# Kernel optimization log

Measured on AMD Instinct MI355X. Metric: run time of the kernel, lower is better.

The kernel has to match this reference:

```python
import jax, jax.numpy as jnp
import numpy as np

NUM_HEADS = 16
NUM_GROUPS = 4
GROUP_SIZE = NUM_HEADS // NUM_GROUPS
EMB_DIM = 1024
HEAD_DIM = EMB_DIM // NUM_HEADS
BLOCK_SIZE = 2048
B, T = 4, 2048


def setup_inputs() -> dict:
    key = jax.random.key(0)
    ks = jax.random.split(key, 7)
    s = 0.02
    x = jax.random.normal(ks[0], (B, T, EMB_DIM), dtype=jnp.float32)
    # nn.Linear weights are [out_features, in_features]; stacked per head/group
    Wq = jax.random.normal(ks[1], (NUM_HEADS, HEAD_DIM, EMB_DIM), dtype=jnp.float32) * s
    Wk = jax.random.normal(ks[2], (NUM_GROUPS, HEAD_DIM, EMB_DIM), dtype=jnp.float32) * s
    Wv = jax.random.normal(ks[3], (NUM_GROUPS, HEAD_DIM, EMB_DIM), dtype=jnp.float32) * s
    Wp = jax.random.normal(ks[4], (EMB_DIM, EMB_DIM), dtype=jnp.float32) * s
    bp = jax.random.normal(ks[5], (EMB_DIM,), dtype=jnp.float32) * s
    return {"x": x, "Wq": Wq, "Wk": Wk, "Wv": Wv, "Wp": Wp, "bp": bp}


def reference(x, Wq, Wk, Wv, Wp, bp):
    # Dropout is treated as identity (eval mode) for a deterministic baseline.
    b, t, c = x.shape
    # per-head queries: [b, t, H, d]
    q = jnp.einsum('btc,hdc->bthd', x, Wq)
    # per-group keys/values: [b, t, G, d]
    k = jnp.einsum('btc,gdc->btgd', x, Wk)
    v = jnp.einsum('btc,gdc->btgd', x, Wv)
    # expand groups to heads: head h uses group h // GROUP_SIZE
    k = jnp.repeat(k, GROUP_SIZE, axis=2)  # [b, t, H, d]
    v = jnp.repeat(v, GROUP_SIZE, axis=2)
    scale = HEAD_DIM ** (-0.5)
    scores = jnp.einsum('bqhd,bkhd->bhqk', q, k) * scale  # [b, H, t, t]
    causal = jnp.tril(jnp.ones((t, t), dtype=bool))
    scores = jnp.where(causal, scores, -jnp.inf)
    p = jax.nn.softmax(scores, axis=-1)
    out = jnp.einsum('bhqk,bkhd->bqhd', p, v)  # [b, t, H, d]
    out = out.reshape(b, t, c)  # concat heads in head-index order
    return out @ Wp.T + bp
```

## Files before the change

### kernel.cpp

```cpp
#include <hip/hip_runtime.h>

typedef unsigned short u16;
typedef __bf16 bf16_t;
typedef bf16_t bf16x8 __attribute__((ext_vector_type(8)));
typedef float f32x4 __attribute__((ext_vector_type(4)));
typedef u16 u16x8 __attribute__((ext_vector_type(8)));

#define T_SZ 2048
#define EMB 1024

static __device__ __forceinline__ u16 f2bf(float f) {
  union { float f; unsigned u; } v; v.f = f;
  return (u16)((v.u + 0x7fffu + ((v.u >> 16) & 1u)) >> 16);
}
static __device__ __forceinline__ unsigned cvtpk(float a, float b) {
  unsigned r;
  asm("v_cvt_pk_bf16_f32 %0, %1, %2" : "=v"(r) : "v"(a), "v"(b));
  return r;
}
static __device__ __forceinline__ void async16(const u16* g, u16* l) {
  typedef const __attribute__((address_space(1))) unsigned int* gp_t;
  typedef __attribute__((address_space(3))) unsigned int* lp_t;
  __builtin_amdgcn_global_load_lds((gp_t)(const void*)g, (lp_t)(void*)l, 16, 0, 0);
}

__global__ __launch_bounds__(256) void cvt_all(
    const float* __restrict__ x,  const float* __restrict__ Wq,
    const float* __restrict__ Wk, const float* __restrict__ Wv,
    const float* __restrict__ Wp, u16* __restrict__ xb, u16* __restrict__ Wqb,
    u16* __restrict__ Wkb, u16* __restrict__ Wvb, u16* __restrict__ Wpb) {
  int bid = blockIdx.x;
  const float* src; u16* dst; int off;
  if (bid < 4096)      { src = x;  dst = xb;  off = bid * 2048; }
  else if (bid < 4608) { src = Wq; dst = Wqb; off = (bid - 4096) * 2048; }
  else if (bid < 4736) { src = Wk; dst = Wkb; off = (bid - 4608) * 2048; }
  else if (bid < 4864) { src = Wv; dst = Wvb; off = (bid - 4736) * 2048; }
  else                 { src = Wp; dst = Wpb; off = (bid - 4864) * 2048; }
  int i = off + threadIdx.x * 8;
  float4 a = *(const float4*)(src + i);
  float4 b = *(const float4*)(src + i + 4);
  u16x8 o;
  o[0] = f2bf(a.x); o[1] = f2bf(a.y); o[2] = f2bf(a.z); o[3] = f2bf(a.w);
  o[4] = f2bf(b.x); o[5] = f2bf(b.y); o[6] = f2bf(b.z); o[7] = f2bf(b.w);
  *(u16x8*)(dst + i) = o;
}

__global__ __launch_bounds__(256) void transpose_v(
    const u16* __restrict__ V, u16* __restrict__ Vt) {
  __shared__ u16 tile[64][72];
  const int tt = blockIdx.x, g = blockIdx.y, b = blockIdx.z;
  const int tid = threadIdx.x;
  {
    const int r = tid >> 2, c = (tid & 3) * 16;
    const u16* src = V + ((size_t)(b * T_SZ + tt * 64 + r)) * 256 + g * 64 + c;
    *(u16x8*)&tile[r][c] = *(const u16x8*)src;
    *(u16x8*)&tile[r][c + 8] = *(const u16x8*)(src + 8);
  }
  __syncthreads();
  {
    const int d = tid >> 2, t0 = (tid & 3) * 16;
    u16x8 o0, o1;
#pragma unroll
    for (int i = 0; i < 8; ++i) { o0[i] = tile[t0 + i][d]; o1[i] = tile[t0 + 8 + i][d]; }
    u16* dst = Vt + ((size_t)((b * 4 + g) * 64 + d)) * T_SZ + tt * 64 + t0;
    *(u16x8*)dst = o0;
    *(u16x8*)(dst + 8) = o1;
  }
}

template <bool OUT_F32>
__device__ __forceinline__ void gemm_body(
    const u16* __restrict__ A, const u16* __restrict__ Bm,
    const float* __restrict__ bias, void* __restrict__ Cv,
    int N, int K, int tm, int tn, float cmul) {
  __shared__ u16 as[128 * 64];
  __shared__ u16 bs[128 * 64];
  const int tid = threadIdx.x;
  const int lane = tid & 63, wv = tid >> 6;
  const int quad = lane >> 4, l16 = lane & 15;
  const int wm = (wv & 1) * 64, wn = (wv >> 1) * 64;
  const int rA = lane >> 3;
  const int cS = ((lane & 7) ^ (rA & 7)) * 8;
  const int x7 = l16 & 7;
  f32x4 acc[4][4] = {};
  for (int k0 = 0; k0 < K; k0 += 64) {
#pragma unroll
    for (int it = 0; it < 4; ++it) {
      int r0 = it * 32 + wv * 8;
      async16(A + (size_t)(tm + r0 + rA) * K + k0 + cS, &as[r0 * 64]);
      async16(Bm + (size_t)(tn + r0 + rA) * K + k0 + cS, &bs[r0 * 64]);
    }
    __syncthreads();
#pragma unroll
    for (int kk = 0; kk < 64; kk += 32) {
      const int cb = kk >> 3;
      bf16x8 af[4], bfr[4];
#pragma unroll
      for (int i = 0; i < 4; ++i)
        af[i] = *(const bf16x8*)&as[(wm + i * 16 + l16) * 64 + (((cb + quad) ^ x7) * 8)];
#pragma unroll
      for (int j = 0; j < 4; ++j)
        bfr[j] = *(const bf16x8*)&bs[(wn + j * 16 + l16) * 64 + (((cb + quad) ^ x7) * 8)];
#pragma unroll
      for (int i = 0; i < 4; ++i)
#pragma unroll
        for (int j = 0; j < 4; ++j)
          acc[i][j] = __builtin_amdgcn_mfma_f32_16x16x32_bf16(af[i], bfr[j], acc[i][j], 0, 0, 0);
    }
    __syncthreads();
  }
#pragma unroll
  for (int i = 0; i < 4; ++i)
#pragma unroll
    for (int j = 0; j < 4; ++j) {
      int col = tn + wn + j * 16 + l16;
      float bv = bias ? bias[col] : 0.0f;
#pragma unroll
      for (int r = 0; r < 4; ++r) {
        int row = tm + wm + i * 16 + quad * 4 + r;
        if (OUT_F32)
          ((float*)Cv)[(size_t)row * N + col] = acc[i][j][r] + bv;
        else
          ((u16*)Cv)[(size_t)row * N + col] = f2bf(acc[i][j][r] * cmul + bv);
      }
    }
}

__global__ __launch_bounds__(256, 2) void gemm_qkv(
    const u16* __restrict__ x, const u16* __restrict__ Wq,
    const u16* __restrict__ Wk, const u16* __restrict__ Wv,
    u16* __restrict__ Qb, u16* __restrict__ Kb, u16* __restrict__ Vb) {
  const int y = blockIdx.y;
  const u16* Bm; u16* C; int N, tn; float cm;
  const float SCALE2 = 0.18033688011112042f;
  if (y < 8)       { Bm = Wq; C = Qb; N = 1024; tn = y * 128;        cm = SCALE2; }
  else if (y < 10) { Bm = Wk; C = Kb; N = 256;  tn = (y - 8) * 128;  cm = 1.0f; }
  else             { Bm = Wv; C = Vb; N = 256;  tn = (y - 10) * 128; cm = 1.0f; }
  gemm_body<false>(x, Bm, nullptr, C, N, 1024, blockIdx.x * 128, tn, cm);
}

__global__ __launch_bounds__(256, 2) void gemm_out(
    const u16* __restrict__ A, const u16* __restrict__ Wp,
    const float* __restrict__ bias, float* __restrict__ C) {
  gemm_body<true>(A, Wp, bias, C, 1024, 1024, blockIdx.x * 128, blockIdx.y * 128, 1.0f);
}

__global__ __launch_bounds__(512, 6) void gqa_attn(
    const u16* __restrict__ Q, const u16* __restrict__ Kg,
    const u16* __restrict__ Vt, u16* __restrict__ O) {
  __shared__ u16 kbuf[3][64 * 64];
  __shared__ u16 vbuf[3][64 * 64];
  __shared__ u16 pls[8][16 * 72];
  const int tid = threadIdx.x;
  const int lane = tid & 63, wv = tid >> 6;
  const int quad = lane >> 4, l16 = lane & 15;
  const int bid = blockIdx.x;
  const int xcd = bid & 7, slot = bid >> 3;
  const int pr = slot & 7, u2 = slot >> 3;
  const int bg = xcd + 8 * (u2 & 1);
  const int b = bg >> 2, g = bg & 3;
  const int h = g * 4 + (u2 >> 1);
  const size_t bT = (size_t)b * T_SZ;
  const int rA = lane >> 3;
  const int cS = ((lane & 7) ^ (rA & 7)) * 8;
  const int x7 = l16 & 7;
  const u16* vtb = Vt + (size_t)((b * 4 + g) * 64) * T_SZ;

#define STAGE(KT, BUF)                                                              \
  do {                                                                              \
    int kb_ = (KT) * 64, r0_ = wv * 8;                   \
    async16(Kg + (bT + kb_ + r0_ + rA) * 256 + g * 64 + cS, &kbuf[BUF][r0_ * 64]);  \
    async16(vtb + (size_t)(r0_ + rA) * T_SZ + kb_ + cS, &vbuf[BUF][r0_ * 64]);      \
    __builtin_amdgcn_sched_barrier(0);                                              \
  } while (0)

  for (int pass = 0; pass < 2; ++pass) {
    const int qt = pass ? pr : 15 - pr;
    const int qstrip = qt * 128 + wv * 16;
    const int nkt = 2 * qt + 2;

    const u16* qp = Q + (bT + qstrip + l16) * EMB + h * 64 + quad * 8;
    const bf16x8 qf0 = *(const bf16x8*)qp;
    const bf16x8 qf1 = *(const bf16x8*)(qp + 32);

    f32x4 o[4] = {};
    float l_p = 0.0f;

    __syncthreads();
    STAGE(0, 0);
    STAGE(1, 1);
    for (int kt = 0; kt < nkt; ++kt) {
      if (kt < nkt - 1) { asm volatile("s_waitcnt vmcnt(2)" ::: "memory"); }
      else              { asm volatile("s_waitcnt vmcnt(0)" ::: "memory"); }
      __builtin_amdgcn_s_barrier();
      if (kt + 2 < nkt) STAGE(kt + 2, (kt + 2) % 3);
      const int cur = kt % 3;
      const int kb = kt * 64;
      const bool act = (kb <= qstrip + 15);

      if (act) {
        f32x4 s4[4];
        __builtin_amdgcn_s_setprio(1);
#pragma unroll
        for (int jn = 0; jn < 4; ++jn) {
          const int rowb = (jn * 16 + l16) * 64;
          bf16x8 kf0 = *(const bf16x8*)&kbuf[cur][rowb + ((quad ^ x7) * 8)];
          bf16x8 kf1 = *(const bf16x8*)&kbuf[cur][rowb + (((4 + quad) ^ x7) * 8)];
          f32x4 a = {};
          a = __builtin_amdgcn_mfma_f32_16x16x32_bf16(kf0, qf0, a, 0, 0, 0);
          a = __builtin_amdgcn_mfma_f32_16x16x32_bf16(kf1, qf1, a, 0, 0, 0);
          s4[jn] = a;
        }
        __builtin_amdgcn_s_setprio(0);
        if (kb + 63 > qstrip) {
          const int qg = qstrip + l16;
#pragma unroll
          for (int jn = 0; jn < 4; ++jn)
#pragma unroll
            for (int r = 0; r < 4; ++r)
              if (kb + jn * 16 + quad * 4 + r > qg) s4[jn][r] = -1e30f;
        }
        float sj[4];
#pragma unroll
        for (int jn = 0; jn < 4; ++jn) {
#pragma unroll
          for (int r = 0; r < 4; ++r) s4[jn][r] = exp2f(s4[jn][r]);
          sj[jn] = (s4[jn][0] + s4[jn][1]) + (s4[jn][2] + s4[jn][3]);
        }
        l_p += (sj[0] + sj[1]) + (sj[2] + sj[3]);
#pragma unroll
        for (int jn = 0; jn < 4; ++jn) {
          uint2 w;
          w.x = cvtpk(s4[jn][0], s4[jn][1]);
          w.y = cvtpk(s4[jn][2], s4[jn][3]);
          *(uint2*)&pls[wv][l16 * 72 + jn * 16 + quad * 4] = w;
        }
        bf16x8 pf0 = *(const bf16x8*)&pls[wv][l16 * 72 + quad * 8];
        bf16x8 pf1 = *(const bf16x8*)&pls[wv][l16 * 72 + 32 + quad * 8];
        __builtin_amdgcn_s_setprio(1);
#pragma unroll
        for (int j = 0; j < 4; ++j) {
          const int rowb = (j * 16 + l16) * 64;
          bf16x8 vf0 = *(const bf16x8*)&vbuf[cur][rowb + ((quad ^ x7) * 8)];
          bf16x8 vf1 = *(const bf16x8*)&vbuf[cur][rowb + (((4 + quad) ^ x7) * 8)];
          o[j] = __builtin_amdgcn_mfma_f32_16x16x32_bf16(pf0, vf0, o[j], 0, 0, 0);
          o[j] = __builtin_amdgcn_mfma_f32_16x16x32_bf16(pf1, vf1, o[j], 0, 0, 0);
        }
        __builtin_amdgcn_s_setprio(0);
      }
    }
    float l_l = l_p;
    l_l += __shfl_xor(l_l, 16);
    l_l += __shfl_xor(l_l, 32);
#pragma unroll
    for (int r = 0; r < 4; ++r) {
      float inv = 1.0f / __shfl(l_l, quad * 4 + r, 16);
      int row = qstrip + quad * 4 + r;
#pragma unroll
      for (int j = 0; j < 4; ++j)
        O[(bT + row) * EMB + h * 64 + j * 16 + l16] = f2bf(o[j][r] * inv);
    }
  }
#undef STAGE
}

extern "C" void kernel_launch(void* const* d_in, const int* in_sizes, int n_in,
                              void* d_out, int out_size, void* d_ws, size_t ws_size,
                              hipStream_t stream) {
  const float* x  = (const float*)d_in[0];
  const float* Wq = (const float*)d_in[1];
  const float* Wk = (const float*)d_in[2];
  const float* Wv = (const float*)d_in[3];
  const float* Wp = (const float*)d_in[4];
  const float* bp = (const float*)d_in[5];
  float* out = (float*)d_out;

  u16* ws = (u16*)d_ws;
  u16* Qb  = ws;
  u16* Kb  = Qb + (size_t)8192 * 1024;
  u16* Vb  = Kb + (size_t)8192 * 256;
  u16* Vtb = Vb + (size_t)8192 * 256;
  u16* xb  = Vtb + (size_t)8192 * 256;
  u16* Wqb = xb + (size_t)8192 * 1024;
  u16* Wkb = Wqb + (size_t)1024 * 1024;
  u16* Wvb = Wkb + (size_t)256 * 1024;
  u16* Wpb = Wvb + (size_t)256 * 1024;
  u16* Ab  = xb;

  cvt_all<<<dim3(5376), 256, 0, stream>>>(x, Wq, Wk, Wv, Wp, xb, Wqb, Wkb, Wvb, Wpb);
  gemm_qkv<<<dim3(64, 12), 256, 0, stream>>>(xb, Wqb, Wkb, Wvb, Qb, Kb, Vb);
  transpose_v<<<dim3(32, 4, 4), 256, 0, stream>>>(Vb, Vtb);
  gqa_attn<<<dim3(512), 512, 0, stream>>>(Qb, Kb, Vtb, Ab);
  gemm_out<<<dim3(64, 8), 256, 0, stream>>>(Ab, Wpb, bp, out);
}
```

Measured before the change: 207.5 us.

## Shrink attention blocks to 64-row query tiles with double buffering and swizzled P

The attention kernel now uses 256-thread blocks, each owning a 64-row query tile, launched as 1024 blocks instead of 512. The triple-buffered K/V pipeline with explicit vmcnt waits becomes a double-buffered one with a __syncthreads per step. The P staging buffer switches from padded rows to an XOR-swizzled layout. Since each wave now always has at least one unmasked key tile, the per-tile activity check goes away, removing idle causal work and improving load balance and occupancy. In exchange, each loaded K/V tile is shared by fewer waves and the shallower pipeline may expose more load latency.

```diff
diff --git a/kernel.cpp b/kernel.cpp
--- a/kernel.cpp
+++ b/kernel.cpp
@@ -145,39 +145,46 @@
   gemm_body<true>(A, Wp, bias, C, 1024, 1024, blockIdx.x * 128, blockIdx.y * 128, 1.0f);
 }
 
-__global__ __launch_bounds__(512, 6) void gqa_attn(
+__global__ __launch_bounds__(256, 4) void gqa_attn(
     const u16* __restrict__ Q, const u16* __restrict__ Kg,
     const u16* __restrict__ Vt, u16* __restrict__ O) {
-  __shared__ u16 kbuf[3][64 * 64];
-  __shared__ u16 vbuf[3][64 * 64];
-  __shared__ u16 pls[8][16 * 72];
+  __shared__ u16 kbuf[2][64 * 64];
+  __shared__ u16 vbuf[2][64 * 64];
+  __shared__ u16 pls[4][16 * 64];
   const int tid = threadIdx.x;
   const int lane = tid & 63, wv = tid >> 6;
   const int quad = lane >> 4, l16 = lane & 15;
   const int bid = blockIdx.x;
-  const int xcd = bid & 7, slot = bid >> 3;
-  const int pr = slot & 7, u2 = slot >> 3;
-  const int bg = xcd + 8 * (u2 & 1);
+  const int xcd = bid & 7;
+  const int slot = (bid >> 3) & 31;
+  const int w = bid >> 8;
+  const int pr = slot & 15;
+  const int bg = xcd + 8 * (w & 1);
   const int b = bg >> 2, g = bg & 3;
-  const int h = g * 4 + (u2 >> 1);
+  const int h = g * 4 + (slot >> 4) + 2 * (w >> 1);
   const size_t bT = (size_t)b * T_SZ;
   const int rA = lane >> 3;
   const int cS = ((lane & 7) ^ (rA & 7)) * 8;
   const int x7 = l16 & 7;
   const u16* vtb = Vt + (size_t)((b * 4 + g) * 64) * T_SZ;
-
-#define STAGE(KT, BUF)                                                              \
-  do {                                                                              \
-    int kb_ = (KT) * 64, r0_ = wv * 8;                   \
-    async16(Kg + (bT + kb_ + r0_ + rA) * 256 + g * 64 + cS, &kbuf[BUF][r0_ * 64]);  \
-    async16(vtb + (size_t)(r0_ + rA) * T_SZ + kb_ + cS, &vbuf[BUF][r0_ * 64]);      \
-    __builtin_amdgcn_sched_barrier(0);                                              \
+  char* pw = (char*)pls + wv * 2048 + l16 * 128;
+
+#define STAGE(KT, BUF)                                                               \
+  do {                                                                               \
+    int kb_ = (KT) * 64, r0_ = wv * 16;                  \
+    async16(Kg + (bT + kb_ + r0_ + rA) * 256 + g * 64 + cS, &kbuf[BUF][r0_ * 64]);   \
+    async16(Kg + (bT + kb_ + r0_ + 8 + rA) * 256 + g * 64 + cS,                      \
+            &kbuf[BUF][(r0_ + 8) * 64]);                                             \
+    async16(vtb + (size_t)(r0_ + rA) * T_SZ + kb_ + cS, &vbuf[BUF][r0_ * 64]);       \
+    async16(vtb + (size_t)(r0_ + 8 + rA) * T_SZ + kb_ + cS,                          \
+            &vbuf[BUF][(r0_ + 8) * 64]);                                             \
+    __builtin_amdgcn_sched_barrier(0);                                               \
   } while (0)
 
   for (int pass = 0; pass < 2; ++pass) {
-    const int qt = pass ? pr : 15 - pr;
-    const int qstrip = qt * 128 + wv * 16;
-    const int nkt = 2 * qt + 2;
+    const int qs = pass ? pr : 31 - pr;
+    const int qstrip = qs * 64 + wv * 16;
+    const int nkt = qs + 1;
 
     const u16* qp = Q + (bT + qstrip + l16) * EMB + h * 64 + quad * 8;
     const bf16x8 qf0 = *(const bf16x8*)qp;
@@ -188,66 +195,60 @@
 
     __syncthreads();
     STAGE(0, 0);
-    STAGE(1, 1);
     for (int kt = 0; kt < nkt; ++kt) {
-      if (kt < nkt - 1) { asm volatile("s_waitcnt vmcnt(2)" ::: "memory"); }
-      else              { asm volatile("s_waitcnt vmcnt(0)" ::: "memory"); }
-      __builtin_amdgcn_s_barrier();
-      if (kt + 2 < nkt) STAGE(kt + 2, (kt + 2) % 3);
-      const int cur = kt % 3;
+      const int cur = kt & 1;
+      __syncthreads();
+      if (kt + 1 < nkt) STAGE(kt + 1, cur ^ 1);
       const int kb = kt * 64;
-      const bool act = (kb <= qstrip + 15);
-
-      if (act) {
-        f32x4 s4[4];
-        __builtin_amdgcn_s_setprio(1);
-#pragma unroll
-        for (int jn = 0; jn < 4; ++jn) {
-          const int rowb = (jn * 16 + l16) * 64;
-          bf16x8 kf0 = *(const bf16x8*)&kbuf[cur][rowb + ((quad ^ x7) * 8)];
-          bf16x8 kf1 = *(const bf16x8*)&kbuf[cur][rowb + (((4 + quad) ^ x7) * 8)];
-          f32x4 a = {};
-          a = __builtin_amdgcn_mfma_f32_16x16x32_bf16(kf0, qf0, a, 0, 0, 0);
-          a = __builtin_amdgcn_mfma_f32_16x16x32_bf16(kf1, qf1, a, 0, 0, 0);
-          s4[jn] = a;
-        }
-        __builtin_amdgcn_s_setprio(0);
-        if (kb + 63 > qstrip) {
-          const int qg = qstrip + l16;
-#pragma unroll
-          for (int jn = 0; jn < 4; ++jn)
-#pragma unroll
-            for (int r = 0; r < 4; ++r)
-              if (kb + jn * 16 + quad * 4 + r > qg) s4[jn][r] = -1e30f;
-        }
-        float sj[4];
-#pragma unroll
-        for (int jn = 0; jn < 4; ++jn) {
-#pragma unroll
-          for (int r = 0; r < 4; ++r) s4[jn][r] = exp2f(s4[jn][r]);
-          sj[jn] = (s4[jn][0] + s4[jn][1]) + (s4[jn][2] + s4[jn][3]);
-        }
-        l_p += (sj[0] + sj[1]) + (sj[2] + sj[3]);
-#pragma unroll
-        for (int jn = 0; jn < 4; ++jn) {
-          uint2 w;
-          w.x = cvtpk(s4[jn][0], s4[jn][1]);
-          w.y = cvtpk(s4[jn][2], s4[jn][3]);
-          *(uint2*)&pls[wv][l16 * 72 + jn * 16 + quad * 4] = w;
-        }
-        bf16x8 pf0 = *(const bf16x8*)&pls[wv][l16 * 72 + quad * 8];
-        bf16x8 pf1 = *(const bf16x8*)&pls[wv][l16 * 72 + 32 + quad * 8];
-        __builtin_amdgcn_s_setprio(1);
-#pragma unroll
-        for (int j = 0; j < 4; ++j) {
-          const int rowb = (j * 16 + l16) * 64;
-          bf16x8 vf0 = *(const bf16x8*)&vbuf[cur][rowb + ((quad ^ x7) * 8)];
-          bf16x8 vf1 = *(const bf16x8*)&vbuf[cur][rowb + (((4 + quad) ^ x7) * 8)];
-          o[j] = __builtin_amdgcn_mfma_f32_16x16x32_bf16(pf0, vf0, o[j], 0, 0, 0);
-          o[j] = __builtin_amdgcn_mfma_f32_16x16x32_bf16(pf1, vf1, o[j], 0, 0, 0);
-        }
-        __builtin_amdgcn_s_setprio(0);
-      }
+
+      f32x4 s4[4];
+      __builtin_amdgcn_s_setprio(1);
+#pragma unroll
+      for (int jn = 0; jn < 4; ++jn) {
+        const int rowb = (jn * 16 + l16) * 64;
+        bf16x8 kf0 = *(const bf16x8*)&kbuf[cur][rowb + ((quad ^ x7) * 8)];
+        bf16x8 kf1 = *(const bf16x8*)&kbuf[cur][rowb + (((4 + quad) ^ x7) * 8)];
+        f32x4 a = {};
+        a = __builtin_amdgcn_mfma_f32_16x16x32_bf16(kf0, qf0, a, 0, 0, 0);
+        a = __builtin_amdgcn_mfma_f32_16x16x32_bf16(kf1, qf1, a, 0, 0, 0);
+        s4[jn] = a;
+      }
+      __builtin_amdgcn_s_setprio(0);
+      if (kb + 63 > qstrip) {
+        const int qg = qstrip + l16;
+#pragma unroll
+        for (int jn = 0; jn < 4; ++jn)
+#pragma unroll
+          for (int r = 0; r < 4; ++r)
+            if (kb + jn * 16 + quad * 4 + r > qg) s4[jn][r] = -1e30f;
+      }
+      float sj[4];
+#pragma unroll
+      for (int jn = 0; jn < 4; ++jn) {
+#pragma unroll
+        for (int r = 0; r < 4; ++r) s4[jn][r] = exp2f(s4[jn][r]);
+        sj[jn] = (s4[jn][0] + s4[jn][1]) + (s4[jn][2] + s4[jn][3]);
+      }
+      l_p += (sj[0] + sj[1]) + (sj[2] + sj[3]);
+#pragma unroll
+      for (int jn = 0; jn < 4; ++jn) {
+        uint2 wq;
+        wq.x = cvtpk(s4[jn][0], s4[jn][1]);
+        wq.y = cvtpk(s4[jn][2], s4[jn][3]);
+        *(uint2*)(pw + ((((jn * 2 + (quad >> 1)) ^ x7) * 16) | ((quad & 1) * 8))) = wq;
+      }
+      bf16x8 pf0 = *(const bf16x8*)(pw + ((quad ^ x7) * 16));
+      bf16x8 pf1 = *(const bf16x8*)(pw + (((4 + quad) ^ x7) * 16));
+      __builtin_amdgcn_s_setprio(1);
+#pragma unroll
+      for (int j = 0; j < 4; ++j) {
+        const int rowb = (j * 16 + l16) * 64;
+        bf16x8 vf0 = *(const bf16x8*)&vbuf[cur][rowb + ((quad ^ x7) * 8)];
+        bf16x8 vf1 = *(const bf16x8*)&vbuf[cur][rowb + (((4 + quad) ^ x7) * 8)];
+        o[j] = __builtin_amdgcn_mfma_f32_16x16x32_bf16(pf0, vf0, o[j], 0, 0, 0);
+        o[j] = __builtin_amdgcn_mfma_f32_16x16x32_bf16(pf1, vf1, o[j], 0, 0, 0);
+      }
+      __builtin_amdgcn_s_setprio(0);
     }
     float l_l = l_p;
     l_l += __shfl_xor(l_l, 16);
@@ -290,6 +291,6 @@
   cvt_all<<<dim3(5376), 256, 0, stream>>>(x, Wq, Wk, Wv, Wp, xb, Wqb, Wkb, Wvb, Wpb);
   gemm_qkv<<<dim3(64, 12), 256, 0, stream>>>(xb, Wqb, Wkb, Wvb, Qb, Kb, Vb);
   transpose_v<<<dim3(32, 4, 4), 256, 0, stream>>>(Vb, Vtb);
-  gqa_attn<<<dim3(512), 512, 0, stream>>>(Qb, Kb, Vtb, Ab);
+  gqa_attn<<<dim3(1024), 256, 0, stream>>>(Qb, Kb, Vtb, Ab);
   gemm_out<<<dim3(64, 8), 256, 0, stream>>>(Ab, Wpb, bp, out);
 }
```

Result: slower. 220.9 us (+6.5%).

## Process two 16-row query tiles per wave to reuse K/V fragments

Applied to the files above, without the earlier changes.

Each wave now handles 32 query rows (two 16-row MFMA tiles) instead of 16, so every K and V fragment read from LDS feeds twice as many MFMAs. The block tiling moves from 128-row to 256-row query strips with a new workgroup-to-strip mapping, replacing the two-pass causal pairing loop. The three-stage LDS ring becomes a double buffer, and launch bounds occupancy drops from 6 to 4. In exchange it uses more registers, gives each wave less lookahead in the pipeline, and produces larger and fewer blocks, which may hurt causal load balance. The launch grid code is not shown, so it is unclear whether it was updated to match the new block count.

```diff
diff --git a/kernel.cpp b/kernel.cpp
--- a/kernel.cpp
+++ b/kernel.cpp
@@ -145,21 +145,24 @@
   gemm_body<true>(A, Wp, bias, C, 1024, 1024, blockIdx.x * 128, blockIdx.y * 128, 1.0f);
 }
 
-__global__ __launch_bounds__(512, 6) void gqa_attn(
+__global__ __launch_bounds__(512, 4) void gqa_attn(
     const u16* __restrict__ Q, const u16* __restrict__ Kg,
     const u16* __restrict__ Vt, u16* __restrict__ O) {
-  __shared__ u16 kbuf[3][64 * 64];
-  __shared__ u16 vbuf[3][64 * 64];
-  __shared__ u16 pls[8][16 * 72];
+  __shared__ u16 kbuf[2][64 * 64];
+  __shared__ u16 vbuf[2][64 * 64];
+  __shared__ u16 pls[8][32 * 72];
   const int tid = threadIdx.x;
   const int lane = tid & 63, wv = tid >> 6;
   const int quad = lane >> 4, l16 = lane & 15;
   const int bid = blockIdx.x;
-  const int xcd = bid & 7, slot = bid >> 3;
-  const int pr = slot & 7, u2 = slot >> 3;
-  const int bg = xcd + 8 * (u2 & 1);
+  const int xcd = bid & 7, slot = (bid >> 3) & 31, w = bid >> 8;
+  const int bg = xcd + 8 * (slot & 1);
   const int b = bg >> 2, g = bg & 3;
-  const int h = g * 4 + (u2 >> 1);
+  const int h = g * 4 + ((slot >> 1) & 3);
+  const int c = (slot >> 3) & 3;
+  const int qs = w ? 7 - c : c;
+  const int nkt = 4 * qs + 4;
+  const int qstrip = qs * 256 + wv * 32;
   const size_t bT = (size_t)b * T_SZ;
   const int rA = lane >> 3;
   const int cS = ((lane & 7) ^ (rA & 7)) * 8;
@@ -174,94 +177,111 @@
     __builtin_amdgcn_sched_barrier(0);                                              \
   } while (0)
 
-  for (int pass = 0; pass < 2; ++pass) {
-    const int qt = pass ? pr : 15 - pr;
-    const int qstrip = qt * 128 + wv * 16;
-    const int nkt = 2 * qt + 2;
-
-    const u16* qp = Q + (bT + qstrip + l16) * EMB + h * 64 + quad * 8;
-    const bf16x8 qf0 = *(const bf16x8*)qp;
-    const bf16x8 qf1 = *(const bf16x8*)(qp + 32);
-
-    f32x4 o[4] = {};
-    float l_p = 0.0f;
-
+  const u16* qpa = Q + (bT + qstrip + l16) * EMB + h * 64 + quad * 8;
+  const u16* qpb = qpa + 16 * EMB;
+  const bf16x8 qf0a = *(const bf16x8*)qpa;
+  const bf16x8 qf1a = *(const bf16x8*)(qpa + 32);
+  const bf16x8 qf0b = *(const bf16x8*)qpb;
+  const bf16x8 qf1b = *(const bf16x8*)(qpb + 32);
+
+  f32x4 oa[4] = {}, ob[4] = {};
+  float lpa = 0.0f, lpb = 0.0f;
+
+  STAGE(0, 0);
+  for (int kt = 0; kt < nkt; ++kt) {
+    const int cur = kt & 1;
     __syncthreads();
-    STAGE(0, 0);
-    STAGE(1, 1);
-    for (int kt = 0; kt < nkt; ++kt) {
-      if (kt < nkt - 1) { asm volatile("s_waitcnt vmcnt(2)" ::: "memory"); }
-      else              { asm volatile("s_waitcnt vmcnt(0)" ::: "memory"); }
-      __builtin_amdgcn_s_barrier();
-      if (kt + 2 < nkt) STAGE(kt + 2, (kt + 2) % 3);
-      const int cur = kt % 3;
-      const int kb = kt * 64;
-      const bool act = (kb <= qstrip + 15);
-
-      if (act) {
-        f32x4 s4[4];
-        __builtin_amdgcn_s_setprio(1);
-#pragma unroll
-        for (int jn = 0; jn < 4; ++jn) {
-          const int rowb = (jn * 16 + l16) * 64;
-          bf16x8 kf0 = *(const bf16x8*)&kbuf[cur][rowb + ((quad ^ x7) * 8)];
-          bf16x8 kf1 = *(const bf16x8*)&kbuf[cur][rowb + (((4 + quad) ^ x7) * 8)];
-          f32x4 a = {};
-          a = __builtin_amdgcn_mfma_f32_16x16x32_bf16(kf0, qf0, a, 0, 0, 0);
-          a = __builtin_amdgcn_mfma_f32_16x16x32_bf16(kf1, qf1, a, 0, 0, 0);
-          s4[jn] = a;
+    if (kt + 1 < nkt) STAGE(kt + 1, cur ^ 1);
+    const int kb = kt * 64;
+    const bool act = (kb <= qstrip + 31);
+
+    if (act) {
+      f32x4 sa[4], sb[4];
+      __builtin_amdgcn_s_setprio(1);
+#pragma unroll
+      for (int jn = 0; jn < 4; ++jn) {
+        const int rowb = (jn * 16 + l16) * 64;
+        bf16x8 kf0 = *(const bf16x8*)&kbuf[cur][rowb + ((quad ^ x7) * 8)];
+        bf16x8 kf1 = *(const bf16x8*)&kbuf[cur][rowb + (((4 + quad) ^ x7) * 8)];
+        f32x4 a = {};
+        a = __builtin_amdgcn_mfma_f32_16x16x32_bf16(kf0, qf0a, a, 0, 0, 0);
+        a = __builtin_amdgcn_mfma_f32_16x16x32_bf16(kf1, qf1a, a, 0, 0, 0);
+        sa[jn] = a;
+        f32x4 bacc = {};
+        bacc = __builtin_amdgcn_mfma_f32_16x16x32_bf16(kf0, qf0b, bacc, 0, 0, 0);
+        bacc = __builtin_amdgcn_mfma_f32_16x16x32_bf16(kf1, qf1b, bacc, 0, 0, 0);
+        sb[jn] = bacc;
+      }
+      __builtin_amdgcn_s_setprio(0);
+      if (kb + 63 > qstrip) {
+        const int qga = qstrip + l16, qgb = qstrip + 16 + l16;
+#pragma unroll
+        for (int jn = 0; jn < 4; ++jn)
+#pragma unroll
+          for (int r = 0; r < 4; ++r) {
+            int kp = kb + jn * 16 + quad * 4 + r;
+            if (kp > qga) sa[jn][r] = -1e30f;
+            if (kp > qgb) sb[jn][r] = -1e30f;
+          }
+      }
+      float sja[4], sjb[4];
+#pragma unroll
+      for (int jn = 0; jn < 4; ++jn) {
+#pragma unroll
+        for (int r = 0; r < 4; ++r) {
+          sa[jn][r] = exp2f(sa[jn][r]);
+          sb[jn][r] = exp2f(sb[jn][r]);
         }
-        __builtin_amdgcn_s_setprio(0);
-        if (kb + 63 > qstrip) {
-          const int qg = qstrip + l16;
-#pragma unroll
-          for (int jn = 0; jn < 4; ++jn)
-#pragma unroll
-            for (int r = 0; r < 4; ++r)
-              if (kb + jn * 16 + quad * 4 + r > qg) s4[jn][r] = -1e30f;
-        }
-        float sj[4];
-#pragma unroll
-        for (int jn = 0; jn < 4; ++jn) {
-#pragma unroll
-          for (int r = 0; r < 4; ++r) s4[jn][r] = exp2f(s4[jn][r]);
-          sj[jn] = (s4[jn][0] + s4[jn][1]) + (s4[jn][2] + s4[jn][3]);
-        }
-        l_p += (sj[0] + sj[1]) + (sj[2] + sj[3]);
-#pragma unroll
-        for (int jn = 0; jn < 4; ++jn) {
-          uint2 w;
-          w.x = cvtpk(s4[jn][0], s4[jn][1]);
-          w.y = cvtpk(s4[jn][2], s4[jn][3]);
-          *(uint2*)&pls[wv][l16 * 72 + jn * 16 + quad * 4] = w;
-        }
-        bf16x8 pf0 = *(const bf16x8*)&pls[wv][l16 * 72 + quad * 8];
-        bf16x8 pf1 = *(const bf16x8*)&pls[wv][l16 * 72 + 32 + quad * 8];
-        __builtin_amdgcn_s_setprio(1);
-#pragma unroll
-        for (int j = 0; j < 4; ++j) {
-          const int rowb = (j * 16 + l16) * 64;
-          bf16x8 vf0 = *(const bf16x8*)&vbuf[cur][rowb + ((quad ^ x7) * 8)];
-          bf16x8 vf1 = *(const bf16x8*)&vbuf[cur][rowb + (((4 + quad) ^ x7) * 8)];
-          o[j] = __builtin_amdgcn_mfma_f32_16x16x32_bf16(pf0, vf0, o[j], 0, 0, 0);
-          o[j] = __builtin_amdgcn_mfma_f32_16x16x32_bf16(pf1, vf1, o[j], 0, 0, 0);
-        }
-        __builtin_amdgcn_s_setprio(0);
-      }
-    }
-    float l_l = l_p;
-    l_l += __shfl_xor(l_l, 16);
-    l_l += __shfl_xor(l_l, 32);
-#pragma unroll
-    for (int r = 0; r < 4; ++r) {
-      float inv = 1.0f / __shfl(l_l, quad * 4 + r, 16);
-      int row = qstrip + quad * 4 + r;
-#pragma unroll
-      for (int j = 0; j < 4; ++j)
-        O[(bT + row) * EMB + h * 64 + j * 16 + l16] = f2bf(o[j][r] * inv);
+        sja[jn] = (sa[jn][0] + sa[jn][1]) + (sa[jn][2] + sa[jn][3]);
+        sjb[jn] = (sb[jn][0] + sb[jn][1]) + (sb[jn][2] + sb[jn][3]);
+      }
+      lpa += (sja[0] + sja[1]) + (sja[2] + sja[3]);
+      lpb += (sjb[0] + sjb[1]) + (sjb[2] + sjb[3]);
+#pragma unroll
+      for (int jn = 0; jn < 4; ++jn) {
+        uint2 wa, wb;
+        wa.x = cvtpk(sa[jn][0], sa[jn][1]); wa.y = cvtpk(sa[jn][2], sa[jn][3]);
+        wb.x = cvtpk(sb[jn][0], sb[jn][1]); wb.y = cvtpk(sb[jn][2], sb[jn][3]);
+        *(uint2*)&pls[wv][l16 * 72 + jn * 16 + quad * 4] = wa;
+        *(uint2*)&pls[wv][(16 + l16) * 72 + jn * 16 + quad * 4] = wb;
+      }
+      bf16x8 pf0a = *(const bf16x8*)&pls[wv][l16 * 72 + quad * 8];
+      bf16x8 pf1a = *(const bf16x8*)&pls[wv][l16 * 72 + 32 + quad * 8];
+      bf16x8 pf0b = *(const bf16x8*)&pls[wv][(16 + l16) * 72 + quad * 8];
+      bf16x8 pf1b = *(const bf16x8*)&pls[wv][(16 + l16) * 72 + 32 + quad * 8];
+      __builtin_amdgcn_s_setprio(1);
+#pragma unroll
+      for (int j = 0; j < 4; ++j) {
+        const int rowb = (j * 16 + l16) * 64;
+        bf16x8 vf0 = *(const bf16x8*)&vbuf[cur][rowb + ((quad ^ x7) * 8)];
+        bf16x8 vf1 = *(const bf16x8*)&vbuf[cur][rowb + (((4 + quad) ^ x7) * 8)];
+        oa[j] = __builtin_amdgcn_mfma_f32_16x16x32_bf16(pf0a, vf0, oa[j], 0, 0, 0);
+        oa[j] = __builtin_amdgcn_mfma_f32_16x16x32_bf16(pf1a, vf1, oa[j], 0, 0, 0);
+        ob[j] = __builtin_amdgcn_mfma_f32_16x16x32_bf16(pf0b, vf0, ob[j], 0, 0, 0);
+        ob[j] = __builtin_amdgcn_mfma_f32_16x16x32_bf16(pf1b, vf1, ob[j], 0, 0, 0);
+      }
+      __builtin_amdgcn_s_setprio(0);
     }
   }
 #undef STAGE
+  float lla = lpa;
+  lla += __shfl_xor(lla, 16);
+  lla += __shfl_xor(lla, 32);
+  float llb = lpb;
+  llb += __shfl_xor(llb, 16);
+  llb += __shfl_xor(llb, 32);
+#pragma unroll
+  for (int r = 0; r < 4; ++r) {
+    float inva = 1.0f / __shfl(lla, quad * 4 + r, 16);
+    float invb = 1.0f / __shfl(llb, quad * 4 + r, 16);
+    int rowa = qstrip + quad * 4 + r;
+    int rowb_ = qstrip + 16 + quad * 4 + r;
+#pragma unroll
+    for (int j = 0; j < 4; ++j) {
+      O[(bT + rowa) * EMB + h * 64 + j * 16 + l16] = f2bf(oa[j][r] * inva);
+      O[(bT + rowb_) * EMB + h * 64 + j * 16 + l16] = f2bf(ob[j][r] * invb);
+    }
+  }
 }
 
 extern "C" void kernel_launch(void* const* d_in, const int* in_sizes, int n_in,
```

Result: slower. 212.6 us (+2.4%).
